# Kernel tuning notes

Measured on AMD Instinct MI355X. Metric: run time of the kernel, lower is better.

Reference implementation:

```python
import jax, jax.numpy as jnp
import numpy as np

B, N, DIM = 32, 1024, 512
HEADS, HEAD_DIM = 8, 64
MLP_HIDDEN = 2048
MAX_DIST = 7
TABLE_SIZE = (2 * MAX_DIST + 1) ** 2  # 225


def setup_inputs() -> dict:
    key = jax.random.key(0)
    ks = jax.random.split(key, 8)
    return {
        "x": jax.random.normal(ks[0], (B, N, DIM), jnp.float32),
        "qkv_w": jax.random.normal(ks[1], (3 * DIM, DIM), jnp.float32) * 0.02,
        "proj_w": jax.random.normal(ks[2], (DIM, DIM), jnp.float32) * 0.02,
        "proj_b": jnp.zeros((DIM,), jnp.float32),
        "mlp_w1": jax.random.normal(ks[3], (MLP_HIDDEN, DIM), jnp.float32) * 0.02,
        "mlp_b1": jnp.zeros((MLP_HIDDEN,), jnp.float32),
        "mlp_w2": jax.random.normal(ks[4], (DIM, MLP_HIDDEN), jnp.float32) * 0.02,
        "mlp_b2": jnp.zeros((DIM,), jnp.float32),
        "norm1_g": jnp.ones((DIM,), jnp.float32),
        "norm1_b": jnp.zeros((DIM,), jnp.float32),
        "norm2_g": jnp.ones((DIM,), jnp.float32),
        "norm2_b": jnp.zeros((DIM,), jnp.float32),
        "bias_table": jax.random.normal(ks[5], (TABLE_SIZE, HEADS), jnp.float32) * 0.02,
        "height": 32,
        "width": 32,
    }


def _rel_pos_index(height, width):
    # exact replication of RelativePositionBias index math (numpy, trace-time)
    coords = np.stack(np.meshgrid(np.arange(height), np.arange(width), indexing="ij"))  # [2,H,W]
    flat = coords.reshape(2, -1)                         # [2,N]
    rel = flat[:, :, None] - flat[:, None, :]            # [2,N,N]
    rel = rel.transpose(1, 2, 0).copy()                  # [N,N,2]
    rel[:, :, 0] += height - 1
    rel[:, :, 1] += width - 1
    rel[:, :, 0] *= 2 * width - 1
    idx = np.clip(rel.sum(-1), 0, TABLE_SIZE - 1)
    return jnp.asarray(idx, jnp.int32)                   # [N,N]


def _layernorm(x, g, b, eps=1e-5):
    mu = x.mean(-1, keepdims=True)
    var = ((x - mu) ** 2).mean(-1, keepdims=True)
    return (x - mu) * jax.lax.rsqrt(var + eps) * g + b


def reference(x, qkv_w, proj_w, proj_b, mlp_w1, mlp_b1, mlp_w2, mlp_b2,
              norm1_g, norm1_b, norm2_g, norm2_b, bias_table, height, width):
    scale = HEAD_DIM ** -0.5
    idx = _rel_pos_index(height, width)
    bias = bias_table[idx]                               # [N,N,heads]
    bias = jnp.transpose(bias, (2, 0, 1))                # [heads,N,N]

    shortcut = x
    h = _layernorm(x, norm1_g, norm1_b)
    qkv = h @ qkv_w.T                                    # [B,N,3*DIM]
    qkv = qkv.reshape(x.shape[0], x.shape[1], 3, HEADS, HEAD_DIM)
    qkv = jnp.transpose(qkv, (2, 0, 3, 1, 4))            # [3,B,h,N,d]
    q, k, v = qkv[0], qkv[1], qkv[2]
    attn = jnp.einsum("bhnd,bhmd->bhnm", q, k) * scale
    attn = attn + bias[None]
    attn = jax.nn.softmax(attn, axis=-1)
    o = jnp.einsum("bhnm,bhmd->bhnd", attn, v)           # [B,h,N,d]
    o = jnp.transpose(o, (0, 2, 1, 3)).reshape(x.shape)  # [B,N,DIM]
    o = o @ proj_w.T + proj_b
    x = shortcut + o

    shortcut = x
    h = _layernorm(x, norm2_g, norm2_b)
    h = jax.nn.gelu(h @ mlp_w1.T + mlp_b1, approximate=False)
    h = h @ mlp_w2.T + mlp_b2
    return shortcut + h
```

## Files before the change

kernel.cpp:

```cpp
#include <hip/hip_runtime.h>

typedef short bf16x8 __attribute__((ext_vector_type(8)));
typedef float f32x4 __attribute__((ext_vector_type(4)));
typedef unsigned short us8 __attribute__((ext_vector_type(8)));
typedef unsigned short us2 __attribute__((ext_vector_type(2)));

__device__ __forceinline__ float bf2f(unsigned short u) {
    union { unsigned i; float f; } v; v.i = ((unsigned)u) << 16; return v.f;
}
__device__ __forceinline__ unsigned short f2bf(float f) {
    union { float f; unsigned i; } v; v.f = f;
    unsigned r = v.i + 0x7fffu + ((v.i >> 16) & 1u);
    return (unsigned short)(r >> 16);
}
__device__ __forceinline__ float ldflex(const void* p, int isf32, long i) {
    return isf32 ? ((const float*)p)[i] : bf2f(((const unsigned short*)p)[i]);
}
__device__ __forceinline__ float gelu_exact(float v) {
    return 0.5f * v * (1.0f + erff(v * 0.70710678118654752f));
}
__device__ __forceinline__ us8 pack8u(const float* s) {
    us8 r;
    #pragma unroll
    for (int i = 0; i < 8; ++i) r[i] = f2bf(s[i]);
    return r;
}
__device__ __forceinline__ unsigned cvtpk_bf16(float lo, float hi) {
    unsigned u;
    asm("v_cvt_pk_bf16_f32 %0, %1, %2" : "=v"(u) : "v"(lo), "v"(hi));
    return u;
}

__device__ __forceinline__ void gld16(const void* g, void* l) {
    typedef __attribute__((address_space(1))) void GV;
    typedef __attribute__((address_space(3))) void LV;
    __builtin_amdgcn_global_load_lds((GV*)g, (LV*)l, 16, 0, 0);
}

struct SniffArgs { const void* p[13]; int n[13]; };

__global__ __launch_bounds__(64) void sniff_all(SniffArgs a, int* __restrict__ flags)
{
    const unsigned short* buf = (const unsigned short*)a.p[blockIdx.x];
    const int n_elems = a.n[blockIdx.x];
    __shared__ int cnt[3];
    if (threadIdx.x < 3) cnt[threadIdx.x] = 0;
    __syncthreads();
    int K = n_elems / 2; if (K > 1024) K = 1024; if (K < 1) K = 1;
    int ins = 0, ne = 0, no = 0;
    for (int i = threadIdx.x; i < K; i += 64) {
        const unsigned lo = buf[2 * i], hi = buf[2 * i + 1];
        const unsigned e = (lo >> 7) & 0xFF;
        ins += (lo != 0 && (e < 90 || e > 160)) ? 1 : 0;
        ne  += (lo != 0);
        no  += (hi != 0);
    }
    atomicAdd(&cnt[0], ins); atomicAdd(&cnt[1], ne); atomicAdd(&cnt[2], no);
    __syncthreads();
    if (threadIdx.x == 0)
        flags[blockIdx.x] = (cnt[0] * 10 > K) || (cnt[1] * 10 < K && cnt[2] * 2 > K);
}

struct CvtArgs { const void* src[7]; void* dst[7]; int fidx[7]; int n[7]; int tobf[7]; };

__global__ __launch_bounds__(256) void convert_params(CvtArgs a, const int* __restrict__ flags)
{
    const int t = blockIdx.y;
    const int i0 = (blockIdx.x * 256 + threadIdx.x) * 8;
    if (i0 >= a.n[t]) return;
    const int f = flags[a.fidx[t]];
    float v[8];
    if (f) {
        const float* s = (const float*)a.src[t] + i0;
        *(f32x4*)&v[0] = *(const f32x4*)s;
        *(f32x4*)&v[4] = *(const f32x4*)(s + 4);
    } else {
        us8 u = *(const us8*)((const unsigned short*)a.src[t] + i0);
        #pragma unroll
        for (int i = 0; i < 8; ++i) v[i] = bf2f(u[i]);
    }
    if (a.tobf[t]) {
        *(us8*)((unsigned short*)a.dst[t] + i0) = pack8u(v);
    } else {
        float* d = (float*)a.dst[t] + i0;
        *(f32x4*)d       = *(f32x4*)&v[0];
        *(f32x4*)(d + 4) = *(f32x4*)&v[4];
    }
}

__global__ __launch_bounds__(256) void gemm_bf16(
    const unsigned short* __restrict__ A, const unsigned short* __restrict__ W,
    void* __restrict__ C, int Nout, int K,
    const float* __restrict__ bias,
    const void* resid, const int* rflag, long resid_row0,
    int act, int out_bf16)
{
    __shared__ unsigned short As[2][128 * 32];
    __shared__ unsigned short Bs[2][128 * 32];
    const int tid  = threadIdx.x;
    const int lane = tid & 63, wv = tid >> 6;
    const int wrow = wv >> 1, wcol = wv & 1;
    const int fm = lane & 15, quad = lane >> 4;

    const int gx = gridDim.x;
    const int nwg = gx * gridDim.y;
    int lin = blockIdx.y * gx + blockIdx.x;
    lin = (lin & 7) * (nwg >> 3) + (lin >> 3);
    const int bm = (lin / gx) * 128, bn = (lin % gx) * 128;

    const int sr = tid >> 2;
    const int sb = (tid & 3) * 16;
    const char* Ab = (const char*)A;
    const char* Wb = (const char*)W;
    const long a0 = ((long)(bm + sr) * K) * 2 + sb;
    const long a1 = ((long)(bm + 64 + sr) * K) * 2 + sb;
    const long b0 = ((long)(bn + sr) * K) * 2 + sb;
    const long b1 = ((long)(bn + 64 + sr) * K) * 2 + sb;
    const int ld = tid * 16;

    auto stage = [&](int bsel, int k0b) {
        char* AD = (char*)As[bsel];
        char* BD = (char*)Bs[bsel];
        gld16(Ab + a0 + k0b, AD + ld);
        gld16(Ab + a1 + k0b, AD + 4096 + ld);
        gld16(Wb + b0 + k0b, BD + ld);
        gld16(Wb + b1 + k0b, BD + 4096 + ld);
    };

    f32x4 acc[4][4] = {};
    const int Kb = K * 2;

    stage(0, 0);
    __syncthreads();
    int cur = 0;
    for (int k0b = 0; k0b < Kb; k0b += 64) {
        if (k0b + 64 < Kb) stage(cur ^ 1, k0b + 64);

        const unsigned short* Ac = As[cur];
        const unsigned short* Bc = Bs[cur];
        bf16x8 af[4], bw[4];
        #pragma unroll
        for (int t = 0; t < 4; ++t) {
            af[t] = *(const bf16x8*)&Ac[(wrow * 64 + t * 16 + fm) * 32 + quad * 8];
            bw[t] = *(const bf16x8*)&Bc[(wcol * 64 + t * 16 + fm) * 32 + quad * 8];
        }
        #pragma unroll
        for (int i = 0; i < 4; ++i)
            #pragma unroll
            for (int j = 0; j < 4; ++j)
                acc[i][j] = __builtin_amdgcn_mfma_f32_16x16x32_bf16(
                                af[i], bw[j], acc[i][j], 0, 0, 0);
        __syncthreads();
        cur ^= 1;
    }

    const int crow0 = bm + wrow * 64, ccol0 = bn + wcol * 64;
    if (out_bf16) {
        unsigned short* Cb = (unsigned short*)C;
        #pragma unroll
        for (int j = 0; j < 4; ++j) {
            const int col = ccol0 + j * 16 + fm;
            const float bv = bias ? bias[col] : 0.0f;
            #pragma unroll
            for (int i = 0; i < 4; ++i)
                #pragma unroll
                for (int r = 0; r < 4; ++r) {
                    const int row = crow0 + i * 16 + quad * 4 + r;
                    float v = acc[i][j][r] + bv;
                    if (act) v = gelu_exact(v);
                    Cb[(long)row * Nout + col] = f2bf(v);
                }
        }
    } else {
        float* Cf = (float*)C;
        const int rfl = resid ? (rflag ? *rflag : 1) : 1;
        #pragma unroll
        for (int j = 0; j < 4; ++j) {
            const int col = ccol0 + j * 16 + fm;
            const float bv = bias ? bias[col] : 0.0f;
            #pragma unroll
            for (int i = 0; i < 4; ++i)
                #pragma unroll
                for (int r = 0; r < 4; ++r) {
                    const int row = crow0 + i * 16 + quad * 4 + r;
                    float v = acc[i][j][r] + bv;
                    if (act)   v = gelu_exact(v);
                    if (resid) v += ldflex(resid, rfl, (resid_row0 + row) * (long)Nout + col);
                    Cf[(long)row * Nout + col] = v;
                }
        }
    }
}

__global__ __launch_bounds__(256) void layernorm_512(
    const void* __restrict__ x, const int* __restrict__ xflag, long row0,
    const void* __restrict__ g, const int* __restrict__ gflag,
    const void* __restrict__ b, const int* __restrict__ bflag,
    unsigned short* __restrict__ o)
{
    const int row = blockIdx.x;
    const int tid = threadIdx.x;
    const int xf = xflag ? *xflag : 1;
    const long base = (row0 + row) * 512 + tid * 2;
    const float vx = ldflex(x, xf, base);
    const float vy = ldflex(x, xf, base + 1);
    float s  = vx + vy;
    float s2 = vx * vx + vy * vy;
    #pragma unroll
    for (int off = 32; off > 0; off >>= 1) {
        s  += __shfl_down(s, off);
        s2 += __shfl_down(s2, off);
    }
    __shared__ float ss[4], ss2[4];
    if ((tid & 63) == 0) { ss[tid >> 6] = s; ss2[tid >> 6] = s2; }
    __syncthreads();
    const float ts   = ss[0] + ss[1] + ss[2] + ss[3];
    const float ts2  = ss2[0] + ss2[1] + ss2[2] + ss2[3];
    const float mean = ts * (1.0f / 512.0f);
    const float var  = ts2 * (1.0f / 512.0f) - mean * mean;
    const float rstd = rsqrtf(var + 1e-5f);
    const int gf = *gflag, bff = *bflag;
    us2 r;
    r[0] = f2bf((vx - mean) * rstd * ldflex(g, gf, tid * 2)     + ldflex(b, bff, tid * 2));
    r[1] = f2bf((vy - mean) * rstd * ldflex(g, gf, tid * 2 + 1) + ldflex(b, bff, tid * 2 + 1));
    *(us2*)(o + (long)row * 512 + tid * 2) = r;
}

__global__ __launch_bounds__(256, 5) void attn_mfma(
    const unsigned short* __restrict__ qkv,
    const void* __restrict__ table, const int* __restrict__ tflag,
    unsigned short* __restrict__ o)
{
    __shared__ unsigned short Ks[512 * 8];
    __shared__ unsigned short Vt[64 * 72];
    __shared__ unsigned short Pl[4][16 * 72];
    __shared__ float Tbh[228];

    const int tid  = threadIdx.x;
    const int lane = tid & 63, wv = tid >> 6;
    const int fm = lane & 15, quad = lane >> 4;

    const int hw    = blockIdx.x + gridDim.x * (blockIdx.y + gridDim.y * blockIdx.z);
    const int total = gridDim.x * gridDim.y * gridDim.z;
    const int lin   = (hw & 7) * (total >> 3) + (hw >> 3);
    const int q0 = (lin & 15) * 64;
    const int h  = (lin >> 4) & 7;
    const int b  = lin >> 7;

    {
        const int tf = *tflag;
        if (tid < 228) {
            const int src = tid > 224 ? 224 : tid;
            Tbh[tid] = ldflex(table, tf, src * 8 + h);
        }
    }

    bf16x8 qa[2];
    {
        const unsigned short* qb = &qkv[(long)((b * 1024 + q0 + wv * 16 + fm) * 3) * 512
                                        + h * 64 + quad * 8];
        qa[0] = *(const bf16x8*)qb;
        qa[1] = *(const bf16x8*)(qb + 32);
    }

    const int qi0   = q0 + wv * 16 + quad * 4;
    const int base0 = 63 * (qi0 >> 5) + (qi0 & 31) + 1984;
    int idxr[4];
    #pragma unroll
    for (int c = 0; c < 4; ++c) {
        const int kj = c * 16 + fm;
        idxr[c] = base0 - (63 * (kj >> 5) + (kj & 31));
    }

    bf16x8 ones8;
    #pragma unroll
    for (int i = 0; i < 8; ++i) ones8[i] = (short)0x3F80;

    const int kc_fm   = tid & 15;
    const int kc_quad = (tid >> 4) & 3;
    const int kc_ch   = (tid >> 6) & 1;
    const int kc_c0   = (tid >> 7) & 1;
    const char* qkvB  = (const char*)qkv;
    long ksrc = (((long)(b * 1024 + kc_c0 * 16 + kc_fm) * 3 + 1) * 512
                 + h * 64 + kc_ch * 32 + kc_quad * 8) * 2;

    const int key_v = tid & 63;
    const int dv    = (tid >> 6) * 16;
    long vsrc = (((long)(b * 1024 + key_v) * 3 + 2) * 512 + h * 64 + dv) * 2;

    char* KsB = (char*)Ks;

    f32x4 acc[4] = {};
    f32x4 accS = {};
    float mrow[4] = {-1e30f, -1e30f, -1e30f, -1e30f};

    us8 kv0 = *(const us8*)(qkvB + ksrc);
    us8 kv1 = *(const us8*)(qkvB + ksrc + 98304);
    us8 vv0 = *(const us8*)(qkvB + vsrc);
    us8 vv1 = *(const us8*)(qkvB + vsrc + 16);

    for (int kt = 0; kt < 16; ++kt) {
        __syncthreads();

        *(us8*)(KsB + tid * 16)        = kv0;
        *(us8*)(KsB + 4096 + tid * 16) = kv1;
        #pragma unroll
        for (int i = 0; i < 8; ++i) Vt[(dv + i) * 72 + key_v]     = vv0[i];
        #pragma unroll
        for (int i = 0; i < 8; ++i) Vt[(dv + 8 + i) * 72 + key_v] = vv1[i];

        if (kt < 15) {
            ksrc += 196608; vsrc += 196608;
            kv0 = *(const us8*)(qkvB + ksrc);
            kv1 = *(const us8*)(qkvB + ksrc + 98304);
            vv0 = *(const us8*)(qkvB + vsrc);
            vv1 = *(const us8*)(qkvB + vsrc + 16);
        }

        asm volatile("s_waitcnt lgkmcnt(0)" ::: "memory");
        __builtin_amdgcn_s_barrier();

        f32x4 sv[4];
        __builtin_amdgcn_s_setprio(1);
        #pragma unroll
        for (int c = 0; c < 4; ++c) {
            f32x4 z = {};
            z = __builtin_amdgcn_mfma_f32_16x16x32_bf16(
                    qa[0], *(const bf16x8*)&Ks[(((c * 2 + 0) * 4 + quad) * 16 + fm) * 8],
                    z, 0, 0, 0);
            z = __builtin_amdgcn_mfma_f32_16x16x32_bf16(
                    qa[1], *(const bf16x8*)&Ks[(((c * 2 + 1) * 4 + quad) * 16 + fm) * 8],
                    z, 0, 0, 0);
            sv[c] = z;
        }
        __builtin_amdgcn_s_setprio(0);

        #pragma unroll
        for (int c = 0; c < 4; ++c) {
            const int i0 = idxr[c] > 224 ? 224 : idxr[c];
            const float* tb = &Tbh[i0];
            idxr[c] -= 126;
            #pragma unroll
            for (int r = 0; r < 4; ++r)
                sv[c][r] = fmaf(sv[c][r], 0.125f, tb[r]);
        }

        float alpha[4];
        #pragma unroll
        for (int r = 0; r < 4; ++r) {
            float mr = fmaxf(fmaxf(sv[0][r], sv[1][r]), fmaxf(sv[2][r], sv[3][r]));
            #pragma unroll
            for (int off = 1; off < 16; off <<= 1) mr = fmaxf(mr, __shfl_xor(mr, off));
            const float mnew = fmaxf(mrow[r], mr);
            alpha[r] = __expf(mrow[r] - mnew);
            mrow[r] = mnew;
            #pragma unroll
            for (int c = 0; c < 4; ++c)
                sv[c][r] = __expf(sv[c][r] - mnew);
        }

        unsigned short* Pw = Pl[wv];
        #pragma unroll
        for (int r = 0; r < 4; ++r) {
            const unsigned u01 = cvtpk_bf16(sv[0][r], sv[1][r]);
            const unsigned u23 = cvtpk_bf16(sv[2][r], sv[3][r]);
            const int row = (quad * 4 + r) * 72;
            Pw[row + fm]      = (unsigned short)u01;
            Pw[row + 16 + fm] = (unsigned short)(u01 >> 16);
            Pw[row + 32 + fm] = (unsigned short)u23;
            Pw[row + 48 + fm] = (unsigned short)(u23 >> 16);
        }

        const bf16x8 ap0 = *(const bf16x8*)&Pw[fm * 72 + quad * 8];
        const bf16x8 ap1 = *(const bf16x8*)&Pw[fm * 72 + 32 + quad * 8];
        __builtin_amdgcn_s_setprio(1);
        #pragma unroll
        for (int c = 0; c < 4; ++c) {
            #pragma unroll
            for (int r = 0; r < 4; ++r) acc[c][r] *= alpha[r];
            acc[c] = __builtin_amdgcn_mfma_f32_16x16x32_bf16(
                        ap0, *(const bf16x8*)&Vt[(c * 16 + fm) * 72 + quad * 8], acc[c], 0, 0, 0);
            acc[c] = __builtin_amdgcn_mfma_f32_16x16x32_bf16(
                        ap1, *(const bf16x8*)&Vt[(c * 16 + fm) * 72 + 32 + quad * 8], acc[c], 0, 0, 0);
        }
        #pragma unroll
        for (int r = 0; r < 4; ++r) accS[r] *= alpha[r];
        accS = __builtin_amdgcn_mfma_f32_16x16x32_bf16(ap0, ones8, accS, 0, 0, 0);
        accS = __builtin_amdgcn_mfma_f32_16x16x32_bf16(ap1, ones8, accS, 0, 0, 0);
        __builtin_amdgcn_s_setprio(0);
    }

    float rinv[4];
    #pragma unroll
    for (int r = 0; r < 4; ++r) rinv[r] = 1.0f / accS[r];
    #pragma unroll
    for (int r = 0; r < 4; ++r) {
        const long ob = (long)(b * 1024 + q0 + wv * 16 + quad * 4 + r) * 512 + h * 64;
        const unsigned u01 = cvtpk_bf16(acc[0][r] * rinv[r], acc[1][r] * rinv[r]);
        const unsigned u23 = cvtpk_bf16(acc[2][r] * rinv[r], acc[3][r] * rinv[r]);
        o[ob + fm]      = (unsigned short)u01;
        o[ob + 16 + fm] = (unsigned short)(u01 >> 16);
        o[ob + 32 + fm] = (unsigned short)u23;
        o[ob + 48 + fm] = (unsigned short)(u23 >> 16);
    }
}

extern "C" void kernel_launch(void* const* d_in, const int* in_sizes, int n_in,
                              void* d_out, int out_size, void* d_ws, size_t ws_size,
                              hipStream_t stream)
{
    (void)n_in; (void)out_size;
    float* out = (float*)d_out;

    constexpr int B = 32, N = 1024;

    int* flags = (int*)d_ws;
    {
        SniffArgs sa;
        for (int t = 0; t < 13; ++t) { sa.p[t] = d_in[t]; sa.n[t] = in_sizes[t]; }
        sniff_all<<<13, 64, 0, stream>>>(sa, flags);
    }

    unsigned short* Wq = (unsigned short*)((char*)d_ws + 256);
    unsigned short* Wp = Wq + 786432;
    unsigned short* W1 = Wp + 262144;
    unsigned short* W2 = W1 + 1048576;
    float* Bp = (float*)(W2 + 1048576);
    float* B1 = Bp + 512;
    float* B2 = B1 + 2048;
    char* scr = (char*)(B2 + 512);
    scr = (char*)(((size_t)scr + 255) & ~(size_t)255);

    {
        CvtArgs ca;
        ca.src[0] = d_in[1]; ca.dst[0] = Wq; ca.fidx[0] = 1; ca.n[0] = 786432;  ca.tobf[0] = 1;
        ca.src[1] = d_in[2]; ca.dst[1] = Wp; ca.fidx[1] = 2; ca.n[1] = 262144;  ca.tobf[1] = 1;
        ca.src[2] = d_in[4]; ca.dst[2] = W1; ca.fidx[2] = 4; ca.n[2] = 1048576; ca.tobf[2] = 1;
        ca.src[3] = d_in[6]; ca.dst[3] = W2; ca.fidx[3] = 6; ca.n[3] = 1048576; ca.tobf[3] = 1;
        ca.src[4] = d_in[3]; ca.dst[4] = Bp; ca.fidx[4] = 3; ca.n[4] = 512;     ca.tobf[4] = 0;
        ca.src[5] = d_in[5]; ca.dst[5] = B1; ca.fidx[5] = 5; ca.n[5] = 2048;    ca.tobf[5] = 0;
        ca.src[6] = d_in[7]; ca.dst[6] = B2; ca.fidx[6] = 7; ca.n[6] = 512;     ca.tobf[6] = 0;
        convert_params<<<dim3(512, 7), 256, 0, stream>>>(ca, flags);
    }

    const size_t fixed = (size_t)(scr - (char*)d_ws);
    const size_t per_batch = (size_t)N * 3072 * 2;
    int bpc = (int)((ws_size - fixed) / per_batch);
    if (bpc < 1) bpc = 1;
    if (bpc > B) bpc = B;

    unsigned short* Ln = (unsigned short*)scr;
    unsigned short* Hd = Ln + (size_t)bpc * N * 512;
    unsigned short* Ao = Hd + (size_t)bpc * N * 2048;

    for (int b0 = 0; b0 < B; b0 += bpc) {
        const int nb   = (B - b0) < bpc ? (B - b0) : bpc;
        const int rows = nb * N;
        const long r0  = (long)b0 * N;

        layernorm_512<<<rows, 256, 0, stream>>>(
            d_in[0], flags + 0, r0, d_in[8], flags + 8, d_in[9], flags + 9, Ln);
        gemm_bf16<<<dim3(12, rows / 128), 256, 0, stream>>>(
            Ln, Wq, Hd, 1536, 512, nullptr, nullptr, nullptr, 0, 0, 1);
        attn_mfma<<<dim3(16, 8, nb), 256, 0, stream>>>(
            Hd, d_in[12], flags + 12, Ao);
        gemm_bf16<<<dim3(4, rows / 128), 256, 0, stream>>>(
            Ao, Wp, out + r0 * 512, 512, 512,
            Bp, d_in[0], flags + 0, r0, 0, 0);
    }

    for (int b0 = 0; b0 < B; b0 += bpc) {
        const int nb   = (B - b0) < bpc ? (B - b0) : bpc;
        const int rows = nb * N;
        const long r0  = (long)b0 * N;

        layernorm_512<<<rows, 256, 0, stream>>>(
            out + r0 * 512, nullptr, 0, d_in[10], flags + 10, d_in[11], flags + 11, Ln);
        gemm_bf16<<<dim3(16, rows / 128), 256, 0, stream>>>(
            Ln, W1, Hd, 2048, 512, B1, nullptr, nullptr, 0, 1, 1);
        gemm_bf16<<<dim3(4, rows / 128), 256, 0, stream>>>(
            Hd, W2, out + r0 * 512, 512, 2048,
            B2, out + r0 * 512, nullptr, 0, 0, 0);
    }
}
```

Baseline: 858.0 us.

## Swizzle GEMM LDS layout and deepen async prefetch with explicit vmcnt waits

```diff
diff --git a/kernel.cpp b/kernel.cpp
--- a/kernel.cpp
+++ b/kernel.cpp
@@ -108,8 +108,8 @@
     lin = (lin & 7) * (nwg >> 3) + (lin >> 3);
     const int bm = (lin / gx) * 128, bn = (lin % gx) * 128;
 
-    const int sr = tid >> 2;
-    const int sb = (tid & 3) * 16;
+    const int sr   = tid >> 2;
+    const int sb   = (((tid & 3) ^ ((sr >> 1) & 3)) * 16);
     const char* Ab = (const char*)A;
     const char* Wb = (const char*)W;
     const long a0 = ((long)(bm + sr) * K) * 2 + sb;
@@ -128,29 +128,43 @@
     };
 
     f32x4 acc[4][4] = {};
-    const int Kb = K * 2;
+    const int nt = (K * 2) / 64;
+
+    const int xsw = (fm >> 1) & 3;
 
     stage(0, 0);
-    __syncthreads();
+    stage(1, 64);
     int cur = 0;
-    for (int k0b = 0; k0b < Kb; k0b += 64) {
-        if (k0b + 64 < Kb) stage(cur ^ 1, k0b + 64);
+    for (int t = 0; t < nt; ++t) {
+        if (t + 1 < nt) { asm volatile("s_waitcnt vmcnt(4)" ::: "memory"); }
+        else            { asm volatile("s_waitcnt vmcnt(0)" ::: "memory"); }
+        __builtin_amdgcn_sched_barrier(0);
+        __builtin_amdgcn_s_barrier();
+        __builtin_amdgcn_sched_barrier(0);
 
         const unsigned short* Ac = As[cur];
         const unsigned short* Bc = Bs[cur];
         bf16x8 af[4], bw[4];
         #pragma unroll
-        for (int t = 0; t < 4; ++t) {
-            af[t] = *(const bf16x8*)&Ac[(wrow * 64 + t * 16 + fm) * 32 + quad * 8];
-            bw[t] = *(const bf16x8*)&Bc[(wcol * 64 + t * 16 + fm) * 32 + quad * 8];
-        }
+        for (int u = 0; u < 4; ++u) {
+            const int qs = (quad ^ xsw) * 8;
+            af[u] = *(const bf16x8*)&Ac[(wrow * 64 + u * 16 + fm) * 32 + qs];
+            bw[u] = *(const bf16x8*)&Bc[(wcol * 64 + u * 16 + fm) * 32 + qs];
+        }
+        __builtin_amdgcn_s_setprio(1);
         #pragma unroll
         for (int i = 0; i < 4; ++i)
             #pragma unroll
             for (int j = 0; j < 4; ++j)
                 acc[i][j] = __builtin_amdgcn_mfma_f32_16x16x32_bf16(
                                 af[i], bw[j], acc[i][j], 0, 0, 0);
-        __syncthreads();
+        __builtin_amdgcn_s_setprio(0);
+
+        asm volatile("s_waitcnt lgkmcnt(0)" ::: "memory");
+        __builtin_amdgcn_sched_barrier(0);
+        __builtin_amdgcn_s_barrier();
+        __builtin_amdgcn_sched_barrier(0);
+        if (t + 2 < nt) stage(cur, (t + 2) * 64);
         cur ^= 1;
     }
 
```

After: 854.3 us. About the same (-0.4%).
